# Kernel optimization log

Hardware: AMD Instinct MI355X
Metric: run time of the kernel (lower is better)

## Reference

```python
import jax, jax.numpy as jnp
import numpy as np

N = 50000          # number of graph nodes
R = 4              # number of relation types (rt_num)
E = 800000         # edges per relation (avg degree 16)
D_IN = 128
D_OUT = 64
EPS = 1e-12        # torch F.normalize eps


def setup_inputs() -> dict:
    key = jax.random.key(0)
    k1, k2, k3, k4, k5 = jax.random.split(key, 5)
    x = jax.random.normal(k1, (N, D_IN), dtype=jnp.float32)
    W = jax.random.normal(k2, (R, D_IN, D_OUT), dtype=jnp.float32)
    b = jnp.zeros((R, D_OUT), dtype=jnp.float32)
    adj_vals = jax.random.uniform(k3, (R, E), dtype=jnp.float32)
    adj_rows = jax.random.randint(k4, (R, E), 0, N, dtype=jnp.int32)
    adj_cols = jax.random.randint(k5, (R, E), 0, N, dtype=jnp.int32)
    return {"x": x, "W": W, "b": b, "adj_vals": adj_vals,
            "adj_rows": adj_rows, "adj_cols": adj_cols, "dropout": 0}


def reference(x, W, b, adj_vals, adj_rows, adj_cols, dropout):
    # dropout == 0 -> F.dropout is the identity; reference is deterministic.
    # Per-relation dense projection: xw[r] = x @ W[r]   -> [R, N, D_OUT]
    xw = jnp.einsum('nd,rdo->rno', x, W)

    def per_relation(xw_r, rows_r, cols_r, vals_r, b_r):
        # sparse adjacency SpMM: out[i] = sum_e vals[e] * xw[cols[e]] for rows[e]==i
        msg = xw_r[cols_r] * vals_r[:, None]                  # [E, D_OUT] gather
        agg = jax.ops.segment_sum(msg, rows_r, num_segments=N)  # [N, D_OUT] scatter-add
        return jax.nn.relu(agg + b_r)                          # bias + act

    outs = jax.vmap(per_relation)(xw, adj_rows, adj_cols, adj_vals, b)  # [R, N, D_OUT]
    total = jnp.sum(outs, axis=0)                               # cross-relation sum
    # L2 normalize over feature dim (torch F.normalize, dim=1)
    norm = jnp.maximum(jnp.linalg.norm(total, axis=1, keepdims=True), EPS)
    return total / norm
```

## Files before the change

### kernel.cpp

```cpp
#include <hip/hip_runtime.h>
#include <hip/hip_bf16.h>
#include <stdint.h>

#define NN 50000
#define DI 128
#define DO 64
#define NE 800000
#define NR 4
#define NB 782
#define NBUCK (NR*NB)
#define PCHUNK 7168
#define PWG ((NE + PCHUNK - 1) / PCHUNK)
#define GEMMB ((NN + 127) / 128)
#define ECAP 1408

typedef short short8 __attribute__((ext_vector_type(8)));
typedef float f32x4  __attribute__((ext_vector_type(4)));
union FragU { uint4 u; short8 s; };

__device__ __forceinline__ uint32_t bfb(float f)
{
    __hip_bfloat16 h = __float2bfloat16(f);
    return (uint32_t)*reinterpret_cast<unsigned short*>(&h);
}

template<int N, int PER, int BLK>
__device__ inline void block_exscan(int* a)
{
    __shared__ int wsum[BLK / 64];
    int tid = threadIdx.x;
    int base = tid * PER;
    int v[PER]; int s = 0;
    #pragma unroll
    for (int j = 0; j < PER; ++j) {
        int idx = base + j;
        int x = (idx < N) ? a[idx] : 0;
        v[j] = s; s += x;
    }
    int lane = tid & 63, wv = tid >> 6;
    int inc = s;
    #pragma unroll
    for (int off = 1; off < 64; off <<= 1) {
        int u = __shfl_up(inc, off);
        if (lane >= off) inc += u;
    }
    if (lane == 63) wsum[wv] = inc;
    __syncthreads();
    int woff = 0;
    for (int w = 0; w < wv; ++w) woff += wsum[w];
    int tb = woff + inc - s;
    #pragma unroll
    for (int j = 0; j < PER; ++j) {
        int idx = base + j;
        if (idx < N) a[idx] = tb + v[j];
    }
}

__global__ __launch_bounds__(256) void prep_kernel(
    const float* __restrict__ W, const int* __restrict__ rows,
    uint16_t* __restrict__ wt, int* __restrict__ gtot)
{
    __shared__ int h[NB];
    int bid = blockIdx.x, tid = threadIdx.x;

    if (bid < 128) {
        int i = bid * 256 + tid;
        int r = i >> 13;
        int k = (i >> 6) & 127;
        int n = i & 63;
        wt[((size_t)(r * DO + n) << 7) + k] = (uint16_t)bfb(W[i]);
    } else {
        int bb = bid - 128;
        int r = bb >> 5, sub = bb & 31;
        for (int i = tid; i < NB; i += 256) h[i] = 0;
        __syncthreads();
        const int4* rr4 = (const int4*)(rows + (size_t)r * NE);
        for (int k = sub * 256 + tid; k < NE / 4; k += 32 * 256) {
            int4 v = rr4[k];
            atomicAdd(&h[v.x >> 6], 1);
            atomicAdd(&h[v.y >> 6], 1);
            atomicAdd(&h[v.z >> 6], 1);
            atomicAdd(&h[v.w >> 6], 1);
        }
        __syncthreads();
        int* gt = gtot + r * NB;
        for (int i = tid; i < NB; i += 256)
            if (h[i]) atomicAdd(&gt[i], h[i]);
    }
}

__global__ __launch_bounds__(512) void bases_kernel(
    const int* __restrict__ gtot, int* __restrict__ gstart,
    int* __restrict__ gcur)
{
    __shared__ int a[NBUCK + 1];
    int tid = threadIdx.x;
    for (int i = tid; i < NBUCK + 1; i += 512) a[i] = (i < NBUCK) ? gtot[i] : 0;
    __syncthreads();
    block_exscan<NBUCK + 1, 7, 512>(a);
    __syncthreads();
    for (int i = tid; i < NBUCK + 1; i += 512) {
        gstart[i] = a[i];
        if (i < NBUCK) gcur[i] = a[i];
    }
}

__global__ __launch_bounds__(512) void gemm_place_kernel(
    const float* __restrict__ x, const uint4* __restrict__ wt4,
    uint16_t* __restrict__ xwb,
    const int* __restrict__ rows, const int* __restrict__ cols,
    const float* __restrict__ vals, int* __restrict__ gcur,
    int2* __restrict__ csr)
{
    __shared__ __align__(16) char smem[63616];
    int tid = threadIdx.x;

    if (blockIdx.x < GEMMB) {
        uint16_t* tile = (uint16_t*)smem;
        int wv = __builtin_amdgcn_readfirstlane(tid >> 6);
        int lane = tid & 63;
        int n0 = blockIdx.x * 128 + wv * 16;
        int m16 = lane & 15, g = lane >> 4;
        bool act = (n0 < NN);

        FragU af[4];
        if (act) {
            const float4* x4 = (const float4*)x;
            size_t rb = ((size_t)(n0 + m16) * DI) >> 2;
            #pragma unroll
            for (int ks = 0; ks < 4; ++ks) {
                float4 f0 = x4[rb + ks * 8 + g * 2];
                float4 f1 = x4[rb + ks * 8 + g * 2 + 1];
                af[ks].u.x = bfb(f0.x) | (bfb(f0.y) << 16);
                af[ks].u.y = bfb(f0.z) | (bfb(f0.w) << 16);
                af[ks].u.z = bfb(f1.x) | (bfb(f1.y) << 16);
                af[ks].u.w = bfb(f1.z) | (bfb(f1.w) << 16);
            }
        }

        int nrows = NN - blockIdx.x * 128; if (nrows > 128) nrows = 128;

        for (int r = 0; r < NR; ++r) {
            if (act) {
                #pragma unroll
                for (int ct = 0; ct < 4; ++ct) {
                    f32x4 acc = {0.f, 0.f, 0.f, 0.f};
                    #pragma unroll
                    for (int ks = 0; ks < 4; ++ks) {
                        FragU b;
                        b.u = wt4[(size_t)((r * DO + ct * 16 + m16) * 16) + ks * 4 + g];
                        acc = __builtin_amdgcn_mfma_f32_16x16x32_bf16(
                            af[ks].s, b.s, acc, 0, 0, 0);
                    }
                    #pragma unroll
                    for (int j = 0; j < 4; ++j)
                        tile[(wv * 16 + g * 4 + j) * 64 + ct * 16 + m16] =
                            (uint16_t)bfb(acc[j]);
                }
            }
            __syncthreads();
            uint4* dst = (uint4*)(xwb + ((size_t)r * NN + blockIdx.x * 128) * 64);
            int tot = nrows * 8;
            for (int i = tid; i < tot; i += 512)
                dst[i] = ((const uint4*)tile)[i];
            __syncthreads();
        }
        return;
    }

    int* lofs  = (int*)smem;
    int* gbase = (int*)(smem + 3136);
    int2* stag = (int2*)(smem + 6272);
    int pb = blockIdx.x - GEMMB;
    int r = pb / PWG;
    int chunk = pb - r * PWG;
    int e0 = chunk * PCHUNK;
    int cnt = NE - e0; if (cnt > PCHUNK) cnt = PCHUNK;
    const int*   rr = rows + (size_t)r * NE + e0;
    const int*   cc = cols + (size_t)r * NE + e0;
    const float* vv = vals + (size_t)r * NE + e0;

    for (int i = tid; i <= NB; i += 512) lofs[i] = 0;
    __syncthreads();
    for (int k = tid; k < cnt; k += 512) atomicAdd(&lofs[rr[k] >> 6], 1);
    __syncthreads();
    block_exscan<NB + 1, 2, 512>(lofs);
    __syncthreads();
    for (int b = tid; b < NB; b += 512) {
        int c = lofs[b + 1] - lofs[b];
        if (c > 0) gbase[b] = atomicAdd(&gcur[r * NB + b], c);
    }
    __syncthreads();
    for (int k = tid; k < cnt; k += 512) {
        int row = rr[k];
        int b = row >> 6;
        int slot = atomicAdd(&lofs[b], 1);
        stag[slot] = make_int2((cc[k] & 0xFFFF) | ((row & 63) << 16) | (b << 22),
                               __float_as_int(vv[k]));
    }
    __syncthreads();
    for (int i = tid; i < cnt; i += 512) {
        int2 t = stag[i];
        unsigned b2 = ((unsigned)t.x) >> 22;
        int start = b2 ? lofs[b2 - 1] : 0;
        csr[gbase[b2] + (i - start)] = t;
    }
}

__global__ __launch_bounds__(512) void spmm2_kernel(
    const uint2* __restrict__ xw2, const int2* __restrict__ csr,
    const int* __restrict__ gstart, const float* __restrict__ bias,
    float* __restrict__ out)
{
    __shared__ int2 ebuf[NR][ECAP];
    __shared__ int rcnt[NR][64];
    __shared__ int rofs[NR][64];
    __shared__ int rcur[NR][64];
    int tid = threadIdx.x, blk = blockIdx.x;
    int wv = __builtin_amdgcn_readfirstlane(tid >> 6);
    int lane = tid & 63;

    if (tid < 256) rcnt[tid >> 6][tid & 63] = 0;
    __syncthreads();

    int sbeg[NR], cnt[NR], scnt[NR];
    int2 ed[NR][3];
    #pragma unroll
    for (int r = 0; r < NR; ++r) {
        int b = r * NB + blk;
        sbeg[r] = gstart[b];
        cnt[r]  = gstart[b + 1] - sbeg[r];
        scnt[r] = cnt[r] > ECAP ? ECAP : cnt[r];
        #pragma unroll
        for (int j = 0; j < 3; ++j) {
            int i = tid + j * 512;
            if (i < scnt[r]) {
                ed[r][j] = csr[sbeg[r] + i];
                atomicAdd(&rcnt[r][(ed[r][j].x >> 16) & 63], 1);
            }
        }
    }
    __syncthreads();

    if (wv < NR) {
        int c = rcnt[wv][lane];
        int inc = c;
        #pragma unroll
        for (int off = 1; off < 64; off <<= 1) {
            int u = __shfl_up(inc, off);
            if (lane >= off) inc += u;
        }
        rofs[wv][lane] = inc - c;
        rcur[wv][lane] = inc - c;
    }
    __syncthreads();

    #pragma unroll
    for (int r = 0; r < NR; ++r) {
        #pragma unroll
        for (int j = 0; j < 3; ++j) {
            int i = tid + j * 512;
            if (i < scnt[r]) {
                int rl = (ed[r][j].x >> 16) & 63;
                int slot = atomicAdd(&rcur[r][rl], 1);
                ebuf[r][slot] = make_int2((r * NN + (ed[r][j].x & 0xFFFF)) << 4,
                                          ed[r][j].y);
            }
        }
    }
    __syncthreads();

    int e4 = lane >> 4, fq = lane & 15;
    float4 br[NR];
    #pragma unroll
    for (int r = 0; r < NR; ++r)
        br[r] = *(const float4*)&bias[r * DO + 4 * fq];

    for (int mi = 0; mi < 8; ++mi) {
        int m = wv * 8 + mi;
        int n = blk * 64 + m;
        if (n >= NN) break;

        int st[NR], dc[NR], dege[NR];
        int maxdeg = 0;
        #pragma unroll
        for (int r = 0; r < NR; ++r) {
            st[r] = rofs[r][m];
            dc[r] = rcnt[r][m];
            dege[r] = (dc[r] + 3) & ~3;
            maxdeg = max(maxdeg, dege[r]);
        }

        float a[NR][4];
        #pragma unroll
        for (int r = 0; r < NR; ++r)
            #pragma unroll
            for (int j = 0; j < 4; ++j) a[r][j] = 0.f;

        float vA[NR]; uint2 uA[NR];
        float vB[NR]; uint2 uB[NR];

        #pragma unroll
        for (int r = 0; r < NR; ++r) {
            if (0 < dege[r]) {
                int e = e4; int ec = e < dc[r] ? e : dc[r] - 1;
                int2 cv = ebuf[r][st[r] + ec];
                vA[r] = (e < dc[r]) ? __int_as_float(cv.y) : 0.f;
                uA[r] = xw2[cv.x + fq];
            } else { vA[r] = 0.f; uA[r] = make_uint2(0u, 0u); }
        }
        for (int k = 0; k < maxdeg; k += 8) {
            #pragma unroll
            for (int r = 0; r < NR; ++r) {
                int kk = k + 4;
                if (kk < dege[r]) {
                    int e = kk + e4; int ec = e < dc[r] ? e : dc[r] - 1;
                    int2 cv = ebuf[r][st[r] + ec];
                    vB[r] = (e < dc[r]) ? __int_as_float(cv.y) : 0.f;
                    uB[r] = xw2[cv.x + fq];
                } else { vB[r] = 0.f; uB[r] = make_uint2(0u, 0u); }
            }
            #pragma unroll
            for (int r = 0; r < NR; ++r) {
                float v = vA[r];
                a[r][0] = fmaf(v, __uint_as_float(uA[r].x << 16),         a[r][0]);
                a[r][1] = fmaf(v, __uint_as_float(uA[r].x & 0xFFFF0000u), a[r][1]);
                a[r][2] = fmaf(v, __uint_as_float(uA[r].y << 16),         a[r][2]);
                a[r][3] = fmaf(v, __uint_as_float(uA[r].y & 0xFFFF0000u), a[r][3]);
            }
            #pragma unroll
            for (int r = 0; r < NR; ++r) {
                int kk = k + 8;
                if (kk < dege[r]) {
                    int e = kk + e4; int ec = e < dc[r] ? e : dc[r] - 1;
                    int2 cv = ebuf[r][st[r] + ec];
                    vA[r] = (e < dc[r]) ? __int_as_float(cv.y) : 0.f;
                    uA[r] = xw2[cv.x + fq];
                } else { vA[r] = 0.f; uA[r] = make_uint2(0u, 0u); }
            }
            #pragma unroll
            for (int r = 0; r < NR; ++r) {
                float v = vB[r];
                a[r][0] = fmaf(v, __uint_as_float(uB[r].x << 16),         a[r][0]);
                a[r][1] = fmaf(v, __uint_as_float(uB[r].x & 0xFFFF0000u), a[r][1]);
                a[r][2] = fmaf(v, __uint_as_float(uB[r].y << 16),         a[r][2]);
                a[r][3] = fmaf(v, __uint_as_float(uB[r].y & 0xFFFF0000u), a[r][3]);
            }
        }

        #pragma unroll
        for (int r = 0; r < NR; ++r) {
            if (cnt[r] > ECAP) {
                for (int i = sbeg[r] + ECAP; i < sbeg[r] + cnt[r]; ++i) {
                    int2 cv = csr[i];
                    int rl = (cv.x >> 16) & 63;
                    float v = (rl == m && lane < 16) ? __int_as_float(cv.y) : 0.f;
                    uint2 u = xw2[(((size_t)r * NN + (cv.x & 0xFFFF)) << 4) + fq];
                    a[r][0] = fmaf(v, __uint_as_float(u.x << 16),         a[r][0]);
                    a[r][1] = fmaf(v, __uint_as_float(u.x & 0xFFFF0000u), a[r][1]);
                    a[r][2] = fmaf(v, __uint_as_float(u.y << 16),         a[r][2]);
                    a[r][3] = fmaf(v, __uint_as_float(u.y & 0xFFFF0000u), a[r][3]);
                }
            }
        }

        float t[4] = {0.f, 0.f, 0.f, 0.f};
        #pragma unroll
        for (int r = 0; r < NR; ++r) {
            #pragma unroll
            for (int j = 0; j < 4; ++j) {
                a[r][j] += __shfl_xor(a[r][j], 16);
                a[r][j] += __shfl_xor(a[r][j], 32);
            }
            t[0] += fmaxf(a[r][0] + br[r].x, 0.f);
            t[1] += fmaxf(a[r][1] + br[r].y, 0.f);
            t[2] += fmaxf(a[r][2] + br[r].z, 0.f);
            t[3] += fmaxf(a[r][3] + br[r].w, 0.f);
        }
        float s2 = t[0]*t[0] + t[1]*t[1] + t[2]*t[2] + t[3]*t[3];
        #pragma unroll
        for (int off = 8; off >= 1; off >>= 1) s2 += __shfl_xor(s2, off);
        float inv = 1.0f / fmaxf(sqrtf(s2), 1e-12f);
        if (lane < 16) {
            float4 o = make_float4(t[0]*inv, t[1]*inv, t[2]*inv, t[3]*inv);
            *(float4*)&out[(size_t)n * DO + 4 * fq] = o;
        }
    }
}

__global__ __launch_bounds__(256) void gemm_kernel(
    const float* __restrict__ x, const float* __restrict__ W,
    __hip_bfloat16* __restrict__ xwb)
{
    __shared__ float Wl[DI * DO];
    for (int i = threadIdx.x; i < DI * DO; i += 256) Wl[i] = W[i];
    __syncthreads();

    int wv   = __builtin_amdgcn_readfirstlane((int)(threadIdx.x >> 6));
    int lane = threadIdx.x & 63;
    int n0   = blockIdx.x * 32 + wv * 8;
    if (n0 >= NN) return;
    int nrows = NN - n0; if (nrows > 8) nrows = 8;

    if (nrows == 8) {
        const float* xr = x + (size_t)n0 * DI;
        float acc[8] = {0.f,0.f,0.f,0.f,0.f,0.f,0.f,0.f};
        #pragma unroll 8
        for (int k = 0; k < DI; ++k) {
            float w = Wl[k * DO + lane];
            #pragma unroll
            for (int rr = 0; rr < 8; ++rr)
                acc[rr] = fmaf(xr[(size_t)rr * DI + k], w, acc[rr]);
        }
        #pragma unroll
        for (int rr = 0; rr < 8; ++rr)
            xwb[(size_t)(n0 + rr) * DO + lane] = __float2bfloat16(acc[rr]);
    } else {
        for (int rr = 0; rr < nrows; ++rr) {
            const float* xr = x + (size_t)(n0 + rr) * DI;
            float acc = 0.f;
            for (int k = 0; k < DI; ++k)
                acc = fmaf(xr[k], Wl[k * DO + lane], acc);
            xwb[(size_t)(n0 + rr) * DO + lane] = __float2bfloat16(acc);
        }
    }
}

__global__ __launch_bounds__(256) void scatter_kernel(
    const __hip_bfloat16* __restrict__ xwb, const float* __restrict__ vals,
    const int* __restrict__ rows, const int* __restrict__ cols,
    float* __restrict__ agg)
{
    const int nPairs = NE / 2;
    int gwave  = (blockIdx.x * 256 + threadIdx.x) >> 6;
    int half   = (threadIdx.x >> 5) & 1;
    int l32    = threadIdx.x & 31;
    int stride = gridDim.x * 4;
    const uint16_t* xw16 = reinterpret_cast<const uint16_t*>(xwb);
    for (int p = gwave; p < nPairs; p += stride) {
        int e = 2 * p + half;
        int row = rows[e]; int col = cols[e]; float v = vals[e];
        uint32_t packed = *reinterpret_cast<const uint32_t*>(
            xw16 + ((size_t)col << 6) + 2 * l32);
        float f0 = __uint_as_float(packed << 16);
        float f1 = __uint_as_float(packed & 0xFFFF0000u);
        float* dst = agg + ((size_t)row << 6) + 2 * l32;
        atomicAdd(dst,     v * f0);
        atomicAdd(dst + 1, v * f1);
    }
}

__global__ __launch_bounds__(256) void accum_kernel(
    float* __restrict__ agg, const float* __restrict__ b,
    float* __restrict__ out, int first)
{
    int i = blockIdx.x * 256 + threadIdx.x;
    if (i >= NN * DO) return;
    float v = agg[i] + b[i & (DO - 1)];
    agg[i] = 0.f;
    v = fmaxf(v, 0.f);
    out[i] = first ? v : (out[i] + v);
}

__global__ __launch_bounds__(256) void norm_kernel(float* __restrict__ out)
{
    int n = (blockIdx.x * 256 + threadIdx.x) >> 6;
    int lane = threadIdx.x & 63;
    if (n >= NN) return;
    size_t idx = (size_t)n * DO + lane;
    float t = out[idx];
    float s = t * t;
    #pragma unroll
    for (int off = 32; off >= 1; off >>= 1) s += __shfl_xor(s, off);
    out[idx] = t / fmaxf(sqrtf(s), 1e-12f);
}

extern "C" void kernel_launch(void* const* d_in, const int* in_sizes, int n_in,
                              void* d_out, int out_size, void* d_ws, size_t ws_size,
                              hipStream_t stream)
{
    const float* x    = (const float*)d_in[0];
    const float* W    = (const float*)d_in[1];
    const float* b    = (const float*)d_in[2];
    const float* vals = (const float*)d_in[3];
    const int*   rows = (const int*)d_in[4];
    const int*   cols = (const int*)d_in[5];
    float* out = (float*)d_out;
    char* ws = (char*)d_ws;

    const size_t O_XW = 0;
    const size_t O_CS = O_XW + (size_t)NR * NN * DO * 2;
    const size_t O_GT = O_CS + (size_t)NR * NE * 8;
    const size_t O_GS = O_GT + (size_t)NBUCK * 4;
    const size_t O_GC = O_GS + (size_t)(NBUCK + 1) * 4;
    const size_t O_WT = O_GC + (size_t)NBUCK * 4;
    const size_t NEED = O_WT + 65536;

    if (ws_size >= NEED) {
        __hip_bfloat16* xwb = (__hip_bfloat16*)(ws + O_XW);
        int2* csr   = (int2*)(ws + O_CS);
        int* gtot   = (int*)(ws + O_GT);
        int* gstart = (int*)(ws + O_GS);
        int* gcur   = (int*)(ws + O_GC);
        uint16_t* wt = (uint16_t*)(ws + O_WT);

        hipMemsetAsync(gtot, 0, (size_t)NBUCK * 4, stream);
        prep_kernel<<<dim3(256), dim3(256), 0, stream>>>(W, rows, wt, gtot);
        bases_kernel<<<dim3(1), dim3(512), 0, stream>>>(gtot, gstart, gcur);
        gemm_place_kernel<<<dim3(GEMMB + PWG * NR), dim3(512), 0, stream>>>(
            x, (const uint4*)wt, (uint16_t*)xwb,
            rows, cols, vals, gcur, csr);
        spmm2_kernel<<<dim3(NB), dim3(512), 0, stream>>>(
            (const uint2*)xwb, csr, gstart, b, out);
    } else {
        __hip_bfloat16* xwb = (__hip_bfloat16*)ws;
        float* agg = (float*)(ws + (size_t)NN * DO * 2);
        hipMemsetAsync(agg, 0, (size_t)NN * DO * 4, stream);
        for (int r = 0; r < NR; ++r) {
            gemm_kernel<<<dim3((NN + 31) / 32), dim3(256), 0, stream>>>(
                x, W + (size_t)r * DI * DO, xwb);
            scatter_kernel<<<dim3(2048), dim3(256), 0, stream>>>(
                xwb, vals + (size_t)r * NE, rows + (size_t)r * NE,
                cols + (size_t)r * NE, agg);
            accum_kernel<<<dim3((NN * DO + 255) / 256), dim3(256), 0, stream>>>(
                agg, b + (size_t)r * DO, out, r == 0);
        }
        norm_kernel<<<dim3((NN * DO + 255) / 256), dim3(256), 0, stream>>>(out);
    }
}
```

Before: 162.7 us.

## Quantize projected features to int8 with per-relation scale for SpMM gather

Tracks a per-relation absolute max during the GEMM via atomicMax, then runs a new pass that converts the bf16 projected features to int8 with a per-relation scale. The SpMM kernel gathers 4-byte int8 rows instead of 8-byte bf16 rows and folds the dequant scale into the edge values. This halves the bytes moved by the random neighbor gather, at the cost of an extra quantization pass over all projected features and a large loss of precision that may break tolerance.

```diff
diff --git a/kernel.cpp b/kernel.cpp
--- a/kernel.cpp
+++ b/kernel.cpp
@@ -107,7 +107,7 @@
 
 __global__ __launch_bounds__(512) void gemm_place_kernel(
     const float* __restrict__ x, const uint4* __restrict__ wt4,
-    uint16_t* __restrict__ xwb,
+    uint16_t* __restrict__ xwb, float* __restrict__ scl,
     const int* __restrict__ rows, const int* __restrict__ cols,
     const float* __restrict__ vals, int* __restrict__ gcur,
     int2* __restrict__ csr)
@@ -141,6 +141,7 @@
         int nrows = NN - blockIdx.x * 128; if (nrows > 128) nrows = 128;
 
         for (int r = 0; r < NR; ++r) {
+            float lmax = 0.f;
             if (act) {
                 #pragma unroll
                 for (int ct = 0; ct < 4; ++ct) {
@@ -153,11 +154,18 @@
                             af[ks].s, b.s, acc, 0, 0, 0);
                     }
                     #pragma unroll
-                    for (int j = 0; j < 4; ++j)
+                    for (int j = 0; j < 4; ++j) {
                         tile[(wv * 16 + g * 4 + j) * 64 + ct * 16 + m16] =
                             (uint16_t)bfb(acc[j]);
+                        lmax = fmaxf(lmax, fabsf(acc[j]));
+                    }
                 }
             }
+            #pragma unroll
+            for (int off = 32; off >= 1; off >>= 1)
+                lmax = fmaxf(lmax, __shfl_xor(lmax, off));
+            if (lane == 0)
+                atomicMax((unsigned int*)(scl + r), __float_as_uint(lmax));
             __syncthreads();
             uint4* dst = (uint4*)(xwb + ((size_t)r * NN + blockIdx.x * 128) * 64);
             int tot = nrows * 8;
@@ -207,9 +215,39 @@
     }
 }
 
+__global__ __launch_bounds__(256) void quant_kernel(
+    const uint4* __restrict__ xwb4, uint2* __restrict__ xq2,
+    const float* __restrict__ scl)
+{
+    const int PER_REL = NN * DO / 8;
+    int r = blockIdx.y;
+    float sinv = 127.0f / fmaxf(scl[r], 1e-20f);
+    int i = blockIdx.x * 256 + threadIdx.x;
+    if (i >= PER_REL) return;
+    uint4 u = xwb4[(size_t)r * PER_REL + i];
+    float f[8];
+    f[0] = __uint_as_float(u.x << 16); f[1] = __uint_as_float(u.x & 0xFFFF0000u);
+    f[2] = __uint_as_float(u.y << 16); f[3] = __uint_as_float(u.y & 0xFFFF0000u);
+    f[4] = __uint_as_float(u.z << 16); f[5] = __uint_as_float(u.z & 0xFFFF0000u);
+    f[6] = __uint_as_float(u.w << 16); f[7] = __uint_as_float(u.w & 0xFFFF0000u);
+    uint32_t q[8];
+    #pragma unroll
+    for (int j = 0; j < 8; ++j) {
+        int t = (int)rintf(f[j] * sinv);
+        t = t > 127 ? 127 : (t < -127 ? -127 : t);
+        q[j] = (uint32_t)t & 0xFFu;
+    }
+    uint2 o;
+    o.x = q[0] | (q[1] << 8) | (q[2] << 16) | (q[3] << 24);
+    o.y = q[4] | (q[5] << 8) | (q[6] << 16) | (q[7] << 24);
+    xq2[(size_t)r * PER_REL + i] = o;
+}
+
+template<int Q8>
 __global__ __launch_bounds__(512) void spmm2_kernel(
-    const uint2* __restrict__ xw2, const int2* __restrict__ csr,
-    const int* __restrict__ gstart, const float* __restrict__ bias,
+    const uint2* __restrict__ xw2, const uint32_t* __restrict__ xq4,
+    const int2* __restrict__ csr, const int* __restrict__ gstart,
+    const float* __restrict__ scl, const float* __restrict__ bias,
     float* __restrict__ out)
 {
     __shared__ int2 ebuf[NR][ECAP];
@@ -220,6 +258,11 @@
     int wv = __builtin_amdgcn_readfirstlane(tid >> 6);
     int lane = tid & 63;
 
+    float sfac[NR];
+    #pragma unroll
+    for (int r = 0; r < NR; ++r)
+        sfac[r] = Q8 ? scl[r] * (1.0f / 127.0f) : 1.0f;
+
     if (tid < 256) rcnt[tid >> 6][tid & 63] = 0;
     __syncthreads();
 
@@ -263,8 +306,9 @@
             if (i < scnt[r]) {
                 int rl = (ed[r][j].x >> 16) & 63;
                 int slot = atomicAdd(&rcur[r][rl], 1);
+                float v = __int_as_float(ed[r][j].y) * sfac[r];
                 ebuf[r][slot] = make_int2((r * NN + (ed[r][j].x & 0xFFFF)) << 4,
-                                          ed[r][j].y);
+                                          __float_as_int(v));
             }
         }
     }
@@ -306,7 +350,7 @@
                 int e = e4; int ec = e < dc[r] ? e : dc[r] - 1;
                 int2 cv = ebuf[r][st[r] + ec];
                 vA[r] = (e < dc[r]) ? __int_as_float(cv.y) : 0.f;
-                uA[r] = xw2[cv.x + fq];
+                if (Q8) uA[r].x = xq4[cv.x + fq]; else uA[r] = xw2[cv.x + fq];
             } else { vA[r] = 0.f; uA[r] = make_uint2(0u, 0u); }
         }
         for (int k = 0; k < maxdeg; k += 8) {
@@ -317,16 +361,24 @@
                     int e = kk + e4; int ec = e < dc[r] ? e : dc[r] - 1;
                     int2 cv = ebuf[r][st[r] + ec];
                     vB[r] = (e < dc[r]) ? __int_as_float(cv.y) : 0.f;
-                    uB[r] = xw2[cv.x + fq];
+                    if (Q8) uB[r].x = xq4[cv.x + fq]; else uB[r] = xw2[cv.x + fq];
                 } else { vB[r] = 0.f; uB[r] = make_uint2(0u, 0u); }
             }
             #pragma unroll
             for (int r = 0; r < NR; ++r) {
                 float v = vA[r];
-                a[r][0] = fmaf(v, __uint_as_float(uA[r].x << 16),         a[r][0]);
-                a[r][1] = fmaf(v, __uint_as_float(uA[r].x & 0xFFFF0000u), a[r][1]);
-                a[r][2] = fmaf(v, __uint_as_float(uA[r].y << 16),         a[r][2]);
-                a[r][3] = fmaf(v, __uint_as_float(uA[r].y & 0xFFFF0000u), a[r][3]);
+                if (Q8) {
+                    uint32_t u = uA[r].x;
+                    a[r][0] = fmaf(v, (float)(((int)(u << 24)) >> 24), a[r][0]);
+                    a[r][1] = fmaf(v, (float)(((int)(u << 16)) >> 24), a[r][1]);
+                    a[r][2] = fmaf(v, (float)(((int)(u <<  8)) >> 24), a[r][2]);
+                    a[r][3] = fmaf(v, (float)(((int)u) >> 24),         a[r][3]);
+                } else {
+                    a[r][0] = fmaf(v, __uint_as_float(uA[r].x << 16),         a[r][0]);
+                    a[r][1] = fmaf(v, __uint_as_float(uA[r].x & 0xFFFF0000u), a[r][1]);
+                    a[r][2] = fmaf(v, __uint_as_float(uA[r].y << 16),         a[r][2]);
+                    a[r][3] = fmaf(v, __uint_as_float(uA[r].y & 0xFFFF0000u), a[r][3]);
+                }
             }
             #pragma unroll
             for (int r = 0; r < NR; ++r) {
@@ -335,16 +387,24 @@
                     int e = kk + e4; int ec = e < dc[r] ? e : dc[r] - 1;
                     int2 cv = ebuf[r][st[r] + ec];
                     vA[r] = (e < dc[r]) ? __int_as_float(cv.y) : 0.f;
-                    uA[r] = xw2[cv.x + fq];
+                    if (Q8) uA[r].x = xq4[cv.x + fq]; else uA[r] = xw2[cv.x + fq];
                 } else { vA[r] = 0.f; uA[r] = make_uint2(0u, 0u); }
             }
             #pragma unroll
             for (int r = 0; r < NR; ++r) {
                 float v = vB[r];
-                a[r][0] = fmaf(v, __uint_as_float(uB[r].x << 16),         a[r][0]);
-                a[r][1] = fmaf(v, __uint_as_float(uB[r].x & 0xFFFF0000u), a[r][1]);
-                a[r][2] = fmaf(v, __uint_as_float(uB[r].y << 16),         a[r][2]);
-                a[r][3] = fmaf(v, __uint_as_float(uB[r].y & 0xFFFF0000u), a[r][3]);
+                if (Q8) {
+                    uint32_t u = uB[r].x;
+                    a[r][0] = fmaf(v, (float)(((int)(u << 24)) >> 24), a[r][0]);
+                    a[r][1] = fmaf(v, (float)(((int)(u << 16)) >> 24), a[r][1]);
+                    a[r][2] = fmaf(v, (float)(((int)(u <<  8)) >> 24), a[r][2]);
+                    a[r][3] = fmaf(v, (float)(((int)u) >> 24),         a[r][3]);
+                } else {
+                    a[r][0] = fmaf(v, __uint_as_float(uB[r].x << 16),         a[r][0]);
+                    a[r][1] = fmaf(v, __uint_as_float(uB[r].x & 0xFFFF0000u), a[r][1]);
+                    a[r][2] = fmaf(v, __uint_as_float(uB[r].y << 16),         a[r][2]);
+                    a[r][3] = fmaf(v, __uint_as_float(uB[r].y & 0xFFFF0000u), a[r][3]);
+                }
             }
         }
 
@@ -354,12 +414,22 @@
                 for (int i = sbeg[r] + ECAP; i < sbeg[r] + cnt[r]; ++i) {
                     int2 cv = csr[i];
                     int rl = (cv.x >> 16) & 63;
-                    float v = (rl == m && lane < 16) ? __int_as_float(cv.y) : 0.f;
-                    uint2 u = xw2[(((size_t)r * NN + (cv.x & 0xFFFF)) << 4) + fq];
-                    a[r][0] = fmaf(v, __uint_as_float(u.x << 16),         a[r][0]);
-                    a[r][1] = fmaf(v, __uint_as_float(u.x & 0xFFFF0000u), a[r][1]);
-                    a[r][2] = fmaf(v, __uint_as_float(u.y << 16),         a[r][2]);
-                    a[r][3] = fmaf(v, __uint_as_float(u.y & 0xFFFF0000u), a[r][3]);
+                    float v = (rl == m && lane < 16)
+                              ? __int_as_float(cv.y) * sfac[r] : 0.f;
+                    int ofs = (int)((((size_t)r * NN + (cv.x & 0xFFFF)) << 4) + fq);
+                    if (Q8) {
+                        uint32_t u = xq4[ofs];
+                        a[r][0] = fmaf(v, (float)(((int)(u << 24)) >> 24), a[r][0]);
+                        a[r][1] = fmaf(v, (float)(((int)(u << 16)) >> 24), a[r][1]);
+                        a[r][2] = fmaf(v, (float)(((int)(u <<  8)) >> 24), a[r][2]);
+                        a[r][3] = fmaf(v, (float)(((int)u) >> 24),         a[r][3]);
+                    } else {
+                        uint2 u = xw2[ofs];
+                        a[r][0] = fmaf(v, __uint_as_float(u.x << 16),         a[r][0]);
+                        a[r][1] = fmaf(v, __uint_as_float(u.x & 0xFFFF0000u), a[r][1]);
+                        a[r][2] = fmaf(v, __uint_as_float(u.y << 16),         a[r][2]);
+                        a[r][3] = fmaf(v, __uint_as_float(u.y & 0xFFFF0000u), a[r][3]);
+                    }
                 }
             }
         }
@@ -491,27 +561,40 @@
     const size_t O_XW = 0;
     const size_t O_CS = O_XW + (size_t)NR * NN * DO * 2;
     const size_t O_GT = O_CS + (size_t)NR * NE * 8;
-    const size_t O_GS = O_GT + (size_t)NBUCK * 4;
+    const size_t O_SC = O_GT + (size_t)NBUCK * 4;
+    const size_t O_GS = O_SC + 16;
     const size_t O_GC = O_GS + (size_t)(NBUCK + 1) * 4;
     const size_t O_WT = O_GC + (size_t)NBUCK * 4;
-    const size_t NEED = O_WT + 65536;
-
-    if (ws_size >= NEED) {
+    const size_t O_XQ = O_WT + 65536;
+    const size_t NEED0 = O_XQ;
+    const size_t NEED1 = O_XQ + (size_t)NR * NN * DO;
+
+    if (ws_size >= NEED0) {
         __hip_bfloat16* xwb = (__hip_bfloat16*)(ws + O_XW);
         int2* csr   = (int2*)(ws + O_CS);
         int* gtot   = (int*)(ws + O_GT);
+        float* scl  = (float*)(ws + O_SC);
         int* gstart = (int*)(ws + O_GS);
         int* gcur   = (int*)(ws + O_GC);
         uint16_t* wt = (uint16_t*)(ws + O_WT);
-
-        hipMemsetAsync(gtot, 0, (size_t)NBUCK * 4, stream);
+        char* xq    = ws + O_XQ;
+        bool q8 = (ws_size >= NEED1);
+
+        hipMemsetAsync(gtot, 0, (size_t)NBUCK * 4 + 16, stream);
         prep_kernel<<<dim3(256), dim3(256), 0, stream>>>(W, rows, wt, gtot);
         bases_kernel<<<dim3(1), dim3(512), 0, stream>>>(gtot, gstart, gcur);
         gemm_place_kernel<<<dim3(GEMMB + PWG * NR), dim3(512), 0, stream>>>(
-            x, (const uint4*)wt, (uint16_t*)xwb,
+            x, (const uint4*)wt, (uint16_t*)xwb, scl,
             rows, cols, vals, gcur, csr);
-        spmm2_kernel<<<dim3(NB), dim3(512), 0, stream>>>(
-            (const uint2*)xwb, csr, gstart, b, out);
+        if (q8) {
+            quant_kernel<<<dim3((NN * DO / 8 + 255) / 256, NR), dim3(256), 0, stream>>>(
+                (const uint4*)xwb, (uint2*)xq, scl);
+            spmm2_kernel<1><<<dim3(NB), dim3(512), 0, stream>>>(
+                (const uint2*)xwb, (const uint32_t*)xq, csr, gstart, scl, b, out);
+        } else {
+            spmm2_kernel<0><<<dim3(NB), dim3(512), 0, stream>>>(
+                (const uint2*)xwb, (const uint32_t*)xq, csr, gstart, scl, b, out);
+        }
     } else {
         __hip_bfloat16* xwb = (__hip_bfloat16*)ws;
         float* agg = (float*)(ws + (size_t)NN * DO * 2);
```

Measured after the change: 292.0 us. +79.5%, slower.
